# Kernel optimization log

Measured on AMD Instinct MI355X. Metric: run time of the kernel, lower is better.

The kernel has to match this reference:

```python
import jax, jax.numpy as jnp
import numpy as np

B, C, W, H = 4, 128, 64, 64
CK = 32  # f/g projection channels


def setup_inputs() -> dict:
    key = jax.random.key(0)
    ks = jax.random.split(key, 8)
    s_in = 1.0 / np.sqrt(C)
    return {
        "x": jax.random.normal(ks[0], (B, C, W, H), dtype=jnp.float32),
        "Wf": jax.random.normal(ks[1], (CK, C), dtype=jnp.float32) * s_in,
        "bf": jnp.zeros((CK,), dtype=jnp.float32),
        "Wg": jax.random.normal(ks[2], (CK, C), dtype=jnp.float32) * s_in,
        "bg": jnp.zeros((CK,), dtype=jnp.float32),
        "Wh": jax.random.normal(ks[3], (C, C), dtype=jnp.float32) * s_in,
        "bh": jnp.zeros((C,), dtype=jnp.float32),
        "gamma": jax.random.normal(ks[4], (1,), dtype=jnp.float32) * 0.1,
    }


def reference(x, Wf, bf, Wg, bg, Wh, bh, gamma):
    b, c, w, h = x.shape
    n = w * h
    xf = x.reshape(b, c, n)                                  # [B,C,N]
    # 1x1 convs == per-pixel linear projections
    f = jnp.einsum('oc,bcn->bon', Wf, xf) + bf[None, :, None]  # [B,32,N]
    g = jnp.einsum('oc,bcn->bon', Wg, xf) + bg[None, :, None]  # [B,32,N]
    v = jnp.einsum('oc,bcn->bon', Wh, xf) + bh[None, :, None]  # [B,C,N]
    # attention = softmax(f^T g) over last dim (g positions), as in the torch code
    att = jax.nn.softmax(jnp.einsum('bkn,bkm->bnm', f, g), axis=-1)  # [B,N,N]
    # self_attention = h @ attention  (contract over f-position axis)
    sa = jnp.einsum('bcn,bnm->bcm', v, att).reshape(b, c, w, h)
    return gamma[0] * sa + x
```

## Files before the change

### kernel.cpp

```cpp
#include <hip/hip_runtime.h>
#include <hip/hip_bf16.h>

#define BB 4
#define CC 128
#define NN 4096
#define CK 32
#define L2E 1.442695040888963f

typedef __attribute__((ext_vector_type(8))) short short8v;
typedef __attribute__((ext_vector_type(4))) float float4v;

__device__ inline ushort f2bf(float f) {
    union { __hip_bfloat16 h; ushort u; } cv;
    cv.h = __float2bfloat16(f);
    return cv.u;
}
__device__ inline float bf2f(ushort u) {
    union { uint u; float f; } cv;
    cv.u = ((uint)u) << 16;
    return cv.f;
}
__device__ inline uint pk2(float lo, float hi) {
    return ((uint)f2bf(lo)) | ((uint)f2bf(hi) << 16);
}
__device__ __forceinline__ void gll16(const void* g, void* l) {
    __builtin_amdgcn_global_load_lds(
        (const __attribute__((address_space(1))) void*)g,
        (__attribute__((address_space(3))) void*)l, 16, 0, 0);
}

__global__ __launch_bounds__(1024) void proj_kernel(
    const float* __restrict__ x,
    const float* __restrict__ Wf, const float* __restrict__ bf,
    const float* __restrict__ Wg, const float* __restrict__ bg,
    const float* __restrict__ Wh, const float* __restrict__ bh,
    const float* __restrict__ gamma,
    ushort* __restrict__ ft, ushort* __restrict__ gt, ushort* __restrict__ vh)
{
    __shared__ float xs[CC][64];
    const int t  = threadIdx.x;
    const int n0 = blockIdx.x * 64;
    const int b  = blockIdx.y;
    const float* xb = x + (size_t)b * CC * NN + n0;

    {
        const int j  = t & 63;
        const int cb = t >> 6;
        #pragma unroll
        for (int i = 0; i < 8; ++i)
            xs[cb + 16 * i][j] = xb[(size_t)(cb + 16 * i) * NN + j];
    }
    __syncthreads();

    const int jq = t & 15;
    const int og = (t >> 4) & 15;
    const int i3 = t >> 8;

    const float* wrow[3];
    float biasv[3];
    int   mode[3], oc[3];
    #pragma unroll
    for (int ii = 0; ii < 3; ++ii) {
        const int i = i3 * 3 + ii;
        if (i < 2)      { oc[ii] = og + 16 * i;       wrow[ii] = Wf + oc[ii] * CC; biasv[ii] = bf[oc[ii]]; mode[ii] = 0; }
        else if (i < 4) { oc[ii] = og + 16 * (i - 2); wrow[ii] = Wg + oc[ii] * CC; biasv[ii] = bg[oc[ii]]; mode[ii] = 1; }
        else            { oc[ii] = og + 16 * (i - 4); wrow[ii] = Wh + oc[ii] * CC; biasv[ii] = bh[oc[ii]]; mode[ii] = 2; }
    }

    float acc[3][4];
    #pragma unroll
    for (int ii = 0; ii < 3; ++ii)
        #pragma unroll
        for (int jj = 0; jj < 4; ++jj) acc[ii][jj] = 0.f;

    #pragma unroll 4
    for (int c4 = 0; c4 < 32; ++c4) {
        float4 wv[3];
        #pragma unroll
        for (int ii = 0; ii < 3; ++ii)
            wv[ii] = *reinterpret_cast<const float4*>(&wrow[ii][c4 * 4]);
        #pragma unroll
        for (int q = 0; q < 4; ++q) {
            const float4 xv = *reinterpret_cast<const float4*>(&xs[c4 * 4 + q][jq * 4]);
            #pragma unroll
            for (int ii = 0; ii < 3; ++ii) {
                const float wq = (q == 0) ? wv[ii].x : (q == 1) ? wv[ii].y
                               : (q == 2) ? wv[ii].z : wv[ii].w;
                acc[ii][0] += wq * xv.x;
                acc[ii][1] += wq * xv.y;
                acc[ii][2] += wq * xv.z;
                acc[ii][3] += wq * xv.w;
            }
        }
    }

    const float sgn = (gamma[0] < 0.f) ? -1.f : 1.f;
    const int n_base = n0 + jq * 4;
    #pragma unroll
    for (int ii = 0; ii < 3; ++ii) {
        if (mode[ii] == 0) {
            #pragma unroll
            for (int jj = 0; jj < 4; ++jj)
                ft[((size_t)b * NN + n_base + jj) * CK + oc[ii]] =
                    f2bf((acc[ii][jj] + biasv[ii]) * L2E);
        } else if (mode[ii] == 1) {
            #pragma unroll
            for (int jj = 0; jj < 4; ++jj)
                gt[((size_t)b * NN + n_base + jj) * CK + oc[ii]] = f2bf(acc[ii][jj] + biasv[ii]);
        } else {
            ushort4 pkv;
            pkv.x = f2bf(sgn * (acc[ii][0] + biasv[ii]));
            pkv.y = f2bf(sgn * (acc[ii][1] + biasv[ii]));
            pkv.z = f2bf(sgn * (acc[ii][2] + biasv[ii]));
            pkv.w = f2bf(sgn * (acc[ii][3] + biasv[ii]));
            *reinterpret_cast<ushort4*>(&vh[((size_t)b * CC + oc[ii]) * NN + n_base]) = pkv;
        }
    }
}

__global__ __launch_bounds__(256) void pass1_kernel(
    const ushort* __restrict__ ft, const ushort* __restrict__ gt,
    float* __restrict__ Dpart)
{
    const int t   = threadIdx.x;
    const int w   = t >> 6;
    const int l   = t & 63;
    const int g16 = l >> 4;
    const int l16 = l & 15;
    const int n0  = blockIdx.x * 64;
    const int b   = blockIdx.y;
    const int mz  = blockIdx.z;

    const ushort* ftb = ft + (size_t)b * NN * CK;
    const ushort* gtb = gt + (size_t)b * NN * CK;

    const short8v afrag = *reinterpret_cast<const short8v*>(
        &ftb[(size_t)(n0 + 16 * w + l16) * CK + 8 * g16]);

    const float4v zf = {0.f, 0.f, 0.f, 0.f};
    float d0 = 0.f, d1 = 0.f, d2 = 0.f, d3 = 0.f;
    const int m0 = mz * 512;

    short8v bfA = *reinterpret_cast<const short8v*>(
        &gtb[(size_t)(m0 + l16) * CK + 8 * g16]);
    #pragma unroll 1
    for (int mt = 0; mt < 32; mt += 2) {
        const short8v bfB = *reinterpret_cast<const short8v*>(
            &gtb[(size_t)(m0 + (mt + 1) * 16 + l16) * CK + 8 * g16]);
        float4v s = __builtin_amdgcn_mfma_f32_16x16x32_bf16(afrag, bfA, zf, 0, 0, 0);
        d0 += __builtin_amdgcn_exp2f(s[0]); d1 += __builtin_amdgcn_exp2f(s[1]);
        d2 += __builtin_amdgcn_exp2f(s[2]); d3 += __builtin_amdgcn_exp2f(s[3]);
        bfA = *reinterpret_cast<const short8v*>(
            &gtb[(size_t)(m0 + (((mt + 2) & 31)) * 16 + l16) * CK + 8 * g16]);
        float4v s2 = __builtin_amdgcn_mfma_f32_16x16x32_bf16(afrag, bfB, zf, 0, 0, 0);
        d0 += __builtin_amdgcn_exp2f(s2[0]); d1 += __builtin_amdgcn_exp2f(s2[1]);
        d2 += __builtin_amdgcn_exp2f(s2[2]); d3 += __builtin_amdgcn_exp2f(s2[3]);
    }
    #pragma unroll
    for (int msk = 1; msk <= 8; msk <<= 1) {
        d0 += __shfl_xor(d0, msk);
        d1 += __shfl_xor(d1, msk);
        d2 += __shfl_xor(d2, msk);
        d3 += __shfl_xor(d3, msk);
    }
    if (l16 < 4) {
        const int n = n0 + 16 * w + 4 * g16 + l16;
        const float v = (l16 == 0) ? d0 : (l16 == 1) ? d1 : (l16 == 2) ? d2 : d3;
        Dpart[((size_t)b * NN + n) * 8 + mz] = v;
    }
}

__global__ __launch_bounds__(256) void reduce_kernel(
    const float* __restrict__ Dpart, float* __restrict__ sc,
    const float* __restrict__ gamma)
{
    const int i = blockIdx.x * 256 + threadIdx.x;
    const float4 a4 = *reinterpret_cast<const float4*>(&Dpart[(size_t)i * 8]);
    const float4 b4 = *reinterpret_cast<const float4*>(&Dpart[(size_t)i * 8 + 4]);
    const float D = (a4.x + a4.y + a4.z + a4.w) + (b4.x + b4.y + b4.z + b4.w);
    sc[i] = fabsf(gamma[0]) / D;
}

__global__ __launch_bounds__(256) void vscale_kernel(
    ushort* __restrict__ vh, const float* __restrict__ sc)
{
    const size_t i8   = (size_t)blockIdx.x * 256 + threadIdx.x;
    const size_t base = i8 * 8;
    const int    n    = (int)(base & (NN - 1));
    const int    b    = (int)(base / ((size_t)CC * NN));

    ushort4 v0 = *reinterpret_cast<const ushort4*>(&vh[base]);
    ushort4 v1 = *reinterpret_cast<const ushort4*>(&vh[base + 4]);
    const float4 s0 = *reinterpret_cast<const float4*>(&sc[(size_t)b * NN + n]);
    const float4 s1 = *reinterpret_cast<const float4*>(&sc[(size_t)b * NN + n + 4]);

    v0.x = f2bf(bf2f(v0.x) * s0.x);
    v0.y = f2bf(bf2f(v0.y) * s0.y);
    v0.z = f2bf(bf2f(v0.z) * s0.z);
    v0.w = f2bf(bf2f(v0.w) * s0.w);
    v1.x = f2bf(bf2f(v1.x) * s1.x);
    v1.y = f2bf(bf2f(v1.y) * s1.y);
    v1.z = f2bf(bf2f(v1.z) * s1.z);
    v1.w = f2bf(bf2f(v1.w) * s1.w);

    *reinterpret_cast<ushort4*>(&vh[base])     = v0;
    *reinterpret_cast<ushort4*>(&vh[base + 4]) = v1;
}

#define WSTR  8192
#define VBUF  4096

__global__ __launch_bounds__(1024) void pass2_kernel(
    const ushort* __restrict__ ft, const ushort* __restrict__ gt,
    const ushort* __restrict__ vh,
    const float* __restrict__ x, float* __restrict__ out)
{
    __shared__ __align__(16) char smem[16 * WSTR];

    const int t   = threadIdx.x;
    const int w   = t >> 6;
    const int l   = t & 63;
    const int g16 = l >> 4;
    const int l16 = l & 15;
    const int ch  = w & 1;
    const int nq  = w >> 1;

    const int bid = blockIdx.x;
    const int xcd = bid & 7;
    const int b   = xcd >> 1;
    const int m0  = ((bid >> 3) + 32 * (xcd & 1)) * 64;

    const ushort* ftb = ft + (size_t)b * NN * CK;
    const ushort* gtb = gt + (size_t)b * NN * CK;
    const ushort* vhb = vh + (size_t)b * CC * NN;

    char* wsm = smem + w * WSTR;

    short8v gfrag[4];
    #pragma unroll
    for (int tm = 0; tm < 4; ++tm)
        gfrag[tm] = *reinterpret_cast<const short8v*>(
            &gtb[(size_t)(m0 + 16 * tm + l16) * CK + 8 * g16]);

    const float4v zf = {0.f, 0.f, 0.f, 0.f};
    float4v acc[4][4];
    #pragma unroll
    for (int tc = 0; tc < 4; ++tc)
        #pragma unroll
        for (int tm = 0; tm < 4; ++tm) acc[tc][tm] = zf;

    const int nbase = nq * 512;
    const int rr = l >> 2, cp = l & 3;

#define STAGE(n0_, bo_) do {                                                   \
    _Pragma("unroll")                                                          \
    for (int j = 0; j < 4; ++j) {                                              \
        const int row = j * 16 + rr;                                           \
        gll16(vhb + (size_t)(64 * ch + row) * NN + (n0_)                       \
                  + (((2 * cp) ^ (row & 6)) << 2),                             \
              wsm + (bo_) + j * 1024);                                         \
    }                                                                          \
} while (0)

    STAGE(nbase, 0);
    asm volatile("s_waitcnt vmcnt(0)" ::: "memory");

    int bo = 0;
    #pragma unroll 1
    for (int st = 0; st < 16; ++st) {
        const int n0 = nbase + st * 32;

        const short8v af0 = *reinterpret_cast<const short8v*>(
            &ftb[(size_t)(n0 + l16) * CK + 8 * g16]);
        const short8v af1 = *reinterpret_cast<const short8v*>(
            &ftb[(size_t)(n0 + 16 + l16) * CK + 8 * g16]);

        if (st < 15) {
            STAGE(n0 + 32, bo ^ VBUF);
            asm volatile("s_waitcnt vmcnt(4)" ::: "memory");
        } else {
            asm volatile("s_waitcnt vmcnt(0)" ::: "memory");
        }

        const char* Vb = wsm + bo;

        union { uint u[4]; short8v s; } pf[4];
        #pragma unroll
        for (int tm = 0; tm < 4; ++tm) {
            float4v s0 = __builtin_amdgcn_mfma_f32_16x16x32_bf16(af0, gfrag[tm], zf, 0, 0, 0);
            float4v s1 = __builtin_amdgcn_mfma_f32_16x16x32_bf16(af1, gfrag[tm], zf, 0, 0, 0);
            pf[tm].u[0] = pk2(__builtin_amdgcn_exp2f(s0[0]), __builtin_amdgcn_exp2f(s0[1]));
            pf[tm].u[1] = pk2(__builtin_amdgcn_exp2f(s0[2]), __builtin_amdgcn_exp2f(s0[3]));
            pf[tm].u[2] = pk2(__builtin_amdgcn_exp2f(s1[0]), __builtin_amdgcn_exp2f(s1[1]));
            pf[tm].u[3] = pk2(__builtin_amdgcn_exp2f(s1[2]), __builtin_amdgcn_exp2f(s1[3]));
        }

        #pragma unroll
        for (int tc = 0; tc < 4; ++tc) {
            const int cl = 16 * tc + l16;
            const uint2 va  = *reinterpret_cast<const uint2*>(
                Vb + cl * 64 + 8 * (g16 ^ (cl & 6)));
            const uint2 vb2 = *reinterpret_cast<const uint2*>(
                Vb + cl * 64 + 8 * ((4 + g16) ^ (cl & 6)));
            union { uint u[4]; short8v s; } av;
            av.u[0] = va.x;  av.u[1] = va.y;
            av.u[2] = vb2.x; av.u[3] = vb2.y;
            #pragma unroll
            for (int tm = 0; tm < 4; ++tm)
                acc[tc][tm] = __builtin_amdgcn_mfma_f32_16x16x32_bf16(av.s, pf[tm].s, acc[tc][tm], 0, 0, 0);
        }
        bo ^= VBUF;
    }
#undef STAGE

    float4v* rl = (float4v*)smem;
    __syncthreads();
    if (nq >= 4) {
        const int slot = (nq - 4) * 2 + ch;
        #pragma unroll
        for (int tc = 0; tc < 4; ++tc)
            #pragma unroll
            for (int tm = 0; tm < 4; ++tm)
                rl[(slot * 16 + tc * 4 + tm) * 64 + l] = acc[tc][tm];
    }
    __syncthreads();
    if (nq < 4) {
        const int slot = nq * 2 + ch;
        #pragma unroll
        for (int tc = 0; tc < 4; ++tc)
            #pragma unroll
            for (int tm = 0; tm < 4; ++tm)
                acc[tc][tm] += rl[(slot * 16 + tc * 4 + tm) * 64 + l];
    }
    __syncthreads();
    if (nq == 2 || nq == 3) {
        const int slot = (nq - 2) * 2 + ch;
        #pragma unroll
        for (int tc = 0; tc < 4; ++tc)
            #pragma unroll
            for (int tm = 0; tm < 4; ++tm)
                rl[(slot * 16 + tc * 4 + tm) * 64 + l] = acc[tc][tm];
    }
    __syncthreads();
    if (nq < 2) {
        const int slot = nq * 2 + ch;
        #pragma unroll
        for (int tc = 0; tc < 4; ++tc)
            #pragma unroll
            for (int tm = 0; tm < 4; ++tm)
                acc[tc][tm] += rl[(slot * 16 + tc * 4 + tm) * 64 + l];
    }
    __syncthreads();
    if (nq == 1) {
        #pragma unroll
        for (int tc = 0; tc < 4; ++tc)
            #pragma unroll
            for (int tm = 0; tm < 4; ++tm)
                rl[(ch * 16 + tc * 4 + tm) * 64 + l] = acc[tc][tm];
    }
    __syncthreads();
    if (nq == 0) {
        const float* xb = x   + (size_t)b * CC * NN;
        float*       ob = out + (size_t)b * CC * NN;
        #pragma unroll
        for (int tc = 0; tc < 4; ++tc) {
            #pragma unroll
            for (int tm = 0; tm < 4; ++tm) {
                float4v s = acc[tc][tm] + rl[(ch * 16 + tc * 4 + tm) * 64 + l];
                const int cb = 64 * ch + 16 * tc + 4 * g16;
                const int m  = m0 + 16 * tm + l16;
                #pragma unroll
                for (int r = 0; r < 4; ++r) {
                    const size_t idx = (size_t)(cb + r) * NN + m;
                    ob[idx] = s[r] + xb[idx];
                }
            }
        }
    }
}

extern "C" void kernel_launch(void* const* d_in, const int* in_sizes, int n_in,
                              void* d_out, int out_size, void* d_ws, size_t ws_size,
                              hipStream_t stream)
{
    const float* x     = (const float*)d_in[0];
    const float* Wf    = (const float*)d_in[1];
    const float* bf    = (const float*)d_in[2];
    const float* Wg    = (const float*)d_in[3];
    const float* bg    = (const float*)d_in[4];
    const float* Wh    = (const float*)d_in[5];
    const float* bh    = (const float*)d_in[6];
    const float* gamma = (const float*)d_in[7];

    ushort* ft = (ushort*)d_ws;
    ushort* gt = ft + (size_t)BB * NN * CK;
    ushort* vh = gt + (size_t)BB * NN * CK;
    float* Dpart = (float*)(vh + (size_t)BB * CC * NN);
    float* sc    = Dpart + (size_t)BB * NN * 8;

    float* out = (float*)d_out;

    proj_kernel<<<dim3(NN / 64, BB), 1024, 0, stream>>>(x, Wf, bf, Wg, bg, Wh, bh, gamma, ft, gt, vh);
    pass1_kernel<<<dim3(NN / 64, BB, 8), 256, 0, stream>>>(ft, gt, Dpart);
    reduce_kernel<<<dim3(BB * NN / 256), 256, 0, stream>>>(Dpart, sc, gamma);
    vscale_kernel<<<dim3(BB * CC * NN / 8 / 256), 256, 0, stream>>>(vh, sc);
    pass2_kernel<<<dim3(256), 1024, 0, stream>>>(ft, gt, vh, x, out);
}
```

Measured before the change: 84.29 us.

## Use bf16 MFMA for the 1x1 projections with prepacked concatenated weights

Adds a small kernel that concatenates Wf/Wg/Wh into one bf16 matrix with the log2e and gamma-sign scaling and biases folded in. The projection kernel now stages x as bf16 in LDS transposed and computes all 192 output channels with 16x16x32 bf16 MFMA instead of scalar FP32 FMAs, using smaller 512-thread blocks over 32 pixels. This targets the ALU-bound projection stage, at the cost of an extra launch, bf16 rounding of x and weights before accumulation, and scattered 2-byte stores for the v output.

After: 82.50 us (median of 3 runs). 1.02x faster.

```diff
diff --git a/kernel.cpp b/kernel.cpp
--- a/kernel.cpp
+++ b/kernel.cpp
@@ -29,91 +29,97 @@
         (__attribute__((address_space(3))) void*)l, 16, 0, 0);
 }
 
-__global__ __launch_bounds__(1024) void proj_kernel(
-    const float* __restrict__ x,
+__global__ __launch_bounds__(512) void wprep_kernel(
     const float* __restrict__ Wf, const float* __restrict__ bf,
     const float* __restrict__ Wg, const float* __restrict__ bg,
     const float* __restrict__ Wh, const float* __restrict__ bh,
     const float* __restrict__ gamma,
+    ushort* __restrict__ Wcat, float* __restrict__ bias_cat)
+{
+    const float sgn = (gamma[0] < 0.f) ? -1.f : 1.f;
+    const int t = blockIdx.x * 512 + threadIdx.x;
+    const int o = t >> 7, c = t & 127;
+    float w, scale;
+    if (o < 32)      { w = Wf[o * 128 + c];        scale = L2E;  }
+    else if (o < 64) { w = Wg[(o - 32) * 128 + c]; scale = 1.f;  }
+    else             { w = Wh[(o - 64) * 128 + c]; scale = sgn;  }
+    Wcat[t] = f2bf(w * scale);
+    if (t < 192) {
+        const float bv = (t < 32) ? bf[t] * L2E
+                       : (t < 64) ? bg[t - 32]
+                                  : bh[t - 64] * sgn;
+        bias_cat[t] = bv;
+    }
+}
+
+__global__ __launch_bounds__(512) void proj_kernel(
+    const float* __restrict__ x, const ushort* __restrict__ Wcat,
+    const float* __restrict__ bias_cat,
     ushort* __restrict__ ft, ushort* __restrict__ gt, ushort* __restrict__ vh)
 {
-    __shared__ float xs[CC][64];
+    __shared__ ushort xs[32][132];
     const int t  = threadIdx.x;
-    const int n0 = blockIdx.x * 64;
+    const int n0 = blockIdx.x * 32;
     const int b  = blockIdx.y;
-    const float* xb = x + (size_t)b * CC * NN + n0;
+    const float* xb = x + (size_t)b * CC * NN;
 
     {
-        const int j  = t & 63;
-        const int cb = t >> 6;
-        #pragma unroll
-        for (int i = 0; i < 8; ++i)
-            xs[cb + 16 * i][j] = xb[(size_t)(cb + 16 * i) * NN + j];
-    }
-    __syncthreads();
-
-    const int jq = t & 15;
-    const int og = (t >> 4) & 15;
-    const int i3 = t >> 8;
-
-    const float* wrow[3];
-    float biasv[3];
-    int   mode[3], oc[3];
-    #pragma unroll
-    for (int ii = 0; ii < 3; ++ii) {
-        const int i = i3 * 3 + ii;
-        if (i < 2)      { oc[ii] = og + 16 * i;       wrow[ii] = Wf + oc[ii] * CC; biasv[ii] = bf[oc[ii]]; mode[ii] = 0; }
-        else if (i < 4) { oc[ii] = og + 16 * (i - 2); wrow[ii] = Wg + oc[ii] * CC; biasv[ii] = bg[oc[ii]]; mode[ii] = 1; }
-        else            { oc[ii] = og + 16 * (i - 4); wrow[ii] = Wh + oc[ii] * CC; biasv[ii] = bh[oc[ii]]; mode[ii] = 2; }
-    }
-
-    float acc[3][4];
-    #pragma unroll
-    for (int ii = 0; ii < 3; ++ii)
-        #pragma unroll
-        for (int jj = 0; jj < 4; ++jj) acc[ii][jj] = 0.f;
-
-    #pragma unroll 4
-    for (int c4 = 0; c4 < 32; ++c4) {
-        float4 wv[3];
-        #pragma unroll
-        for (int ii = 0; ii < 3; ++ii)
-            wv[ii] = *reinterpret_cast<const float4*>(&wrow[ii][c4 * 4]);
-        #pragma unroll
-        for (int q = 0; q < 4; ++q) {
-            const float4 xv = *reinterpret_cast<const float4*>(&xs[c4 * 4 + q][jq * 4]);
-            #pragma unroll
-            for (int ii = 0; ii < 3; ++ii) {
-                const float wq = (q == 0) ? wv[ii].x : (q == 1) ? wv[ii].y
-                               : (q == 2) ? wv[ii].z : wv[ii].w;
-                acc[ii][0] += wq * xv.x;
-                acc[ii][1] += wq * xv.y;
-                acc[ii][2] += wq * xv.z;
-                acc[ii][3] += wq * xv.w;
-            }
-        }
-    }
-
-    const float sgn = (gamma[0] < 0.f) ? -1.f : 1.f;
-    const int n_base = n0 + jq * 4;
-    #pragma unroll
-    for (int ii = 0; ii < 3; ++ii) {
-        if (mode[ii] == 0) {
-            #pragma unroll
-            for (int jj = 0; jj < 4; ++jj)
-                ft[((size_t)b * NN + n_base + jj) * CK + oc[ii]] =
-                    f2bf((acc[ii][jj] + biasv[ii]) * L2E);
-        } else if (mode[ii] == 1) {
-            #pragma unroll
-            for (int jj = 0; jj < 4; ++jj)
-                gt[((size_t)b * NN + n_base + jj) * CK + oc[ii]] = f2bf(acc[ii][jj] + biasv[ii]);
+        const int nl = t & 31, cg = t >> 5;
+        #pragma unroll
+        for (int i = 0; i < 8; ++i) {
+            const int c = cg + 16 * i;
+            xs[nl][c] = f2bf(xb[(size_t)c * NN + n0 + nl]);
+        }
+    }
+    __syncthreads();
+
+    const int w   = t >> 6;
+    const int l   = t & 63;
+    const int g16 = l >> 4;
+    const int l16 = l & 15;
+    const int og  = w >> 1;
+    const int nh  = w & 1;
+
+    const float4v zf = {0.f, 0.f, 0.f, 0.f};
+    float4v acc[3];
+    #pragma unroll
+    for (int tt = 0; tt < 3; ++tt) acc[tt] = zf;
+
+    #pragma unroll
+    for (int kt = 0; kt < 4; ++kt) {
+        const short8v bfr = *reinterpret_cast<const short8v*>(
+            &xs[nh * 16 + l16][32 * kt + 8 * g16]);
+        #pragma unroll
+        for (int tt = 0; tt < 3; ++tt) {
+            const short8v afr = *reinterpret_cast<const short8v*>(
+                &Wcat[(size_t)(48 * og + 16 * tt + l16) * 128 + 32 * kt + 8 * g16]);
+            acc[tt] = __builtin_amdgcn_mfma_f32_16x16x32_bf16(afr, bfr, acc[tt], 0, 0, 0);
+        }
+    }
+
+    const int n = n0 + nh * 16 + l16;
+    #pragma unroll
+    for (int tt = 0; tt < 3; ++tt) {
+        const int ob = 48 * og + 16 * tt + 4 * g16;
+        const float4 b4 = *reinterpret_cast<const float4*>(&bias_cat[ob]);
+        const float v0 = acc[tt][0] + b4.x;
+        const float v1 = acc[tt][1] + b4.y;
+        const float v2 = acc[tt][2] + b4.z;
+        const float v3 = acc[tt][3] + b4.w;
+        if (ob < 32) {
+            ushort4 pk;
+            pk.x = f2bf(v0); pk.y = f2bf(v1); pk.z = f2bf(v2); pk.w = f2bf(v3);
+            *reinterpret_cast<ushort4*>(&ft[((size_t)b * NN + n) * CK + ob]) = pk;
+        } else if (ob < 64) {
+            ushort4 pk;
+            pk.x = f2bf(v0); pk.y = f2bf(v1); pk.z = f2bf(v2); pk.w = f2bf(v3);
+            *reinterpret_cast<ushort4*>(&gt[((size_t)b * NN + n) * CK + (ob - 32)]) = pk;
         } else {
-            ushort4 pkv;
-            pkv.x = f2bf(sgn * (acc[ii][0] + biasv[ii]));
-            pkv.y = f2bf(sgn * (acc[ii][1] + biasv[ii]));
-            pkv.z = f2bf(sgn * (acc[ii][2] + biasv[ii]));
-            pkv.w = f2bf(sgn * (acc[ii][3] + biasv[ii]));
-            *reinterpret_cast<ushort4*>(&vh[((size_t)b * CC + oc[ii]) * NN + n_base]) = pkv;
+            const int c = ob - 64;
+            vh[((size_t)b * CC + c + 0) * NN + n] = f2bf(v0);
+            vh[((size_t)b * CC + c + 1) * NN + n] = f2bf(v1);
+            vh[((size_t)b * CC + c + 2) * NN + n] = f2bf(v2);
+            vh[((size_t)b * CC + c + 3) * NN + n] = f2bf(v3);
         }
     }
 }
@@ -397,10 +403,13 @@
     ushort* vh = gt + (size_t)BB * NN * CK;
     float* Dpart = (float*)(vh + (size_t)BB * CC * NN);
     float* sc    = Dpart + (size_t)BB * NN * 8;
+    float* bias_cat = sc + (size_t)BB * NN;
+    ushort* Wcat = (ushort*)(bias_cat + 192);
 
     float* out = (float*)d_out;
 
-    proj_kernel<<<dim3(NN / 64, BB), 1024, 0, stream>>>(x, Wf, bf, Wg, bg, Wh, bh, gamma, ft, gt, vh);
+    wprep_kernel<<<dim3(48), 512, 0, stream>>>(Wf, bf, Wg, bg, Wh, bh, gamma, Wcat, bias_cat);
+    proj_kernel<<<dim3(NN / 32, BB), 512, 0, stream>>>(x, Wcat, bias_cat, ft, gt, vh);
     pass1_kernel<<<dim3(NN / 64, BB, 8), 256, 0, stream>>>(ft, gt, Dpart);
     reduce_kernel<<<dim3(BB * NN / 256), 256, 0, stream>>>(Dpart, sc, gamma);
     vscale_kernel<<<dim3(BB * CC * NN / 8 / 256), 256, 0, stream>>>(vh, sc);
```
